# Kernel optimization log

Hardware: AMD Instinct MI355X
Metric: run time of the kernel (lower is better)

The kernel has to match this reference:

```python
import jax, jax.numpy as jnp
import numpy as np

B, S, E, H = 64, 256, 512, 1024  # batch, seq_len, embed, hidden (dis_size=[512,1024,1024])


def _ln(x, g, b, eps=1e-5):
    # LayerNorm over last axis; x: [..., 3, H], g/b: [3, H] (per-gate affine)
    m = x.mean(-1, keepdims=True)
    v = ((x - m) ** 2).mean(-1, keepdims=True)
    return (x - m) * jax.lax.rsqrt(v + eps) * g + b


def _gru_cell(h, x, Wih, Whh, bih, bhh, gig, gib, ghg, ghb):
    Bsz = x.shape[0]
    Hh = h.shape[1]
    pi = _ln((x @ Wih.T + bih).reshape(Bsz, 3, Hh), gig, gib)
    ph = _ln((h @ Whh.T + bhh).reshape(Bsz, 3, Hh), ghg, ghb)
    r = jax.nn.sigmoid(pi[:, 0] + ph[:, 0])
    z = jax.nn.sigmoid(pi[:, 1] + ph[:, 1])
    n = jnp.tanh(pi[:, 2] + r * ph[:, 2])
    return (1.0 - z) * n + z * h


def _unroll(x, layers, W_out, b_out):
    # x: [B, S, E] -> scalar score per batch element from last hidden state
    xs = jnp.swapaxes(x, 0, 1)  # [S, B, E]
    for (Wih, Whh, bih, bhh, gig, gib, ghg, ghb) in layers:
        h0 = jnp.zeros((x.shape[0], Whh.shape[1]), x.dtype)

        def step(h, xt, Wih=Wih, Whh=Whh, bih=bih, bhh=bhh, gig=gig, gib=gib, ghg=ghg, ghb=ghb):
            h2 = _gru_cell(h, xt, Wih, Whh, bih, bhh, gig, gib, ghg, ghb)
            return h2, h2

        _, xs = jax.lax.scan(step, h0, xs)  # xs becomes [S, B, H]
    return (xs[-1] @ W_out.T + b_out)[:, 0]  # [B]


def setup_inputs() -> dict:
    key = jax.random.key(0)
    ks = jax.random.split(key, 12)
    sizes = [(E, H), (H, H)]  # (input_size, hidden_size) per layer
    inp = {
        "generated_data": jax.random.normal(ks[0], (B, S, E), jnp.float32),
        "true_data": jax.random.normal(ks[1], (B, S, E), jnp.float32),
    }
    for li, (ins, hs) in enumerate(sizes):
        k = jax.random.split(ks[2 + li], 4)
        inp[f"W_ih{li}"] = jax.random.normal(k[0], (3 * hs, ins), jnp.float32) * 0.02
        inp[f"W_hh{li}"] = jax.random.normal(k[1], (3 * hs, hs), jnp.float32) * 0.02
        inp[f"b_ih{li}"] = jnp.zeros((3 * hs,), jnp.float32)
        inp[f"b_hh{li}"] = jnp.zeros((3 * hs,), jnp.float32)
        inp[f"gi_g{li}"] = jnp.ones((3, hs), jnp.float32)
        inp[f"gi_b{li}"] = jnp.zeros((3, hs), jnp.float32)
        inp[f"gh_g{li}"] = jnp.ones((3, hs), jnp.float32)
        inp[f"gh_b{li}"] = jnp.zeros((3, hs), jnp.float32)
    inp["W_out"] = jax.random.normal(ks[10], (1, H), jnp.float32) * 0.02
    inp["b_out"] = jnp.zeros((1,), jnp.float32)
    return inp


def reference(generated_data, true_data,
              W_ih0, W_hh0, b_ih0, b_hh0, gi_g0, gi_b0, gh_g0, gh_b0,
              W_ih1, W_hh1, b_ih1, b_hh1, gi_g1, gi_b1, gh_g1, gh_b1,
              W_out, b_out):
    layers = [
        (W_ih0, W_hh0, b_ih0, b_hh0, gi_g0, gi_b0, gh_g0, gh_b0),
        (W_ih1, W_hh1, b_ih1, b_hh1, gi_g1, gi_b1, gh_g1, gh_b1),
    ]
    true_labels = _unroll(true_data, layers, W_out, b_out)
    gen_labels = _unroll(generated_data, layers, W_out, b_out)
    discriminator_loss = -true_labels.mean() + gen_labels.mean()
    generator_loss = -gen_labels.mean()
    return (discriminator_loss, generator_loss)
```

## Files before the change

kernel.cpp:

```cpp
#include <hip/hip_runtime.h>
#include <math.h>

#define NCH   128
#define SLEN  256
#define HDIM  1024
#define N3    3072

typedef __attribute__((ext_vector_type(8))) __bf16 bf16x8;
typedef __attribute__((ext_vector_type(4))) float  f32x4;

__device__ __forceinline__ f32x4 mfma_bf16(bf16x8 a, bf16x8 b, f32x4 c) {
  return __builtin_amdgcn_mfma_f32_16x16x32_bf16(a, b, c, 0, 0, 0);
}

__device__ __forceinline__ float ld_sc1_f32(const float* p) {
  return __hip_atomic_load(p, __ATOMIC_RELAXED, __HIP_MEMORY_SCOPE_AGENT);
}
__device__ __forceinline__ void st_sc1_f32(float* p, float v) {
  __hip_atomic_store(p, v, __ATOMIC_RELAXED, __HIP_MEMORY_SCOPE_AGENT);
}
__device__ __forceinline__ unsigned long long ld_sc1_u64(const unsigned long long* p) {
  return __hip_atomic_load(p, __ATOMIC_RELAXED, __HIP_MEMORY_SCOPE_AGENT);
}
__device__ __forceinline__ void st_sc1_u32(unsigned int* p, unsigned int v) {
  __hip_atomic_store(p, v, __ATOMIC_RELAXED, __HIP_MEMORY_SCOPE_AGENT);
}
__device__ __forceinline__ int ld_sc1_i32(const int* p) {
  return __hip_atomic_load(p, __ATOMIC_RELAXED, __HIP_MEMORY_SCOPE_AGENT);
}
__device__ __forceinline__ void st_sc1_i32(int* p, int v) {
  __hip_atomic_store(p, v, __ATOMIC_RELAXED, __HIP_MEMORY_SCOPE_AGENT);
}

__global__ __launch_bounds__(256) void prep(
    const float* __restrict__ Whh0, const float* __restrict__ Whh1,
    const float* __restrict__ Wih1, const float* __restrict__ Wih0,
    __bf16* __restrict__ Whh0h, __bf16* __restrict__ Whh0l,
    __bf16* __restrict__ Whh1h, __bf16* __restrict__ Whh1l,
    __bf16* __restrict__ Wih1h, __bf16* __restrict__ Wih1l,
    __bf16* __restrict__ Wih0h, __bf16* __restrict__ Wih0l,
    unsigned int* __restrict__ Hpk,
    int* __restrict__ flags)
{
  const int NB = N3 * HDIM;
  const int NS = N3 * 512;
  int i = blockIdx.x * 256 + threadIdx.x;
  const float* src; __bf16 *dh, *dl; int j;
  if (i < NB)            { src = Whh0; dh = Whh0h; dl = Whh0l; j = i; }
  else if (i < 2 * NB)   { src = Whh1; dh = Whh1h; dl = Whh1l; j = i - NB; }
  else if (i < 3 * NB)   { src = Wih1; dh = Wih1h; dl = Wih1l; j = i - 2 * NB; }
  else if (i < 3 * NB + NS) { src = Wih0; dh = Wih0h; dl = Wih0l; j = i - 3 * NB; }
  else if (i < 3 * NB + NS + 2 * NCH * HDIM) { Hpk[i - 3 * NB - NS] = 0u; return; }
  else if (i < 3 * NB + NS + 2 * NCH * HDIM + 512) {
    flags[i - 3 * NB - NS - 2 * NCH * HDIM] = 0; return;
  }
  else return;
  float x = src[j];
  __bf16 h = (__bf16)x;
  dh[j] = h;
  dl[j] = (__bf16)(x - (float)h);
}

__global__ __launch_bounds__(256) void xproj_mfma(
    const float* __restrict__ A0, const float* __restrict__ A1,
    int chainsA0, int strideChain, int t0, int K, int lTc,
    const __bf16* __restrict__ Wh, const __bf16* __restrict__ Wl,
    const float* __restrict__ bias, float* __restrict__ out)
{
  __shared__ __bf16 Ah[4][128][8];
  __shared__ __bf16 Al[4][128][8];
  const int tid  = threadIdx.x;
  const int n0   = blockIdx.x * 128;
  const int row0 = blockIdx.y * 128;
  const int lane = tid & 63;
  const int wv   = tid >> 6;
  const int q    = lane >> 4;
  const int c15  = lane & 15;
  const int m_off = wv * 32;
  const int sr  = tid >> 1;
  const int sq0 = (tid & 1) * 2;
  const int sk  = (tid & 1) * 16;
  const int r     = row0 + sr;
  const int chain = r >> lTc;
  const int dt    = r & ((1 << lTc) - 1);
  const float* aptr = (chain < chainsA0)
      ? (A0 + ((size_t)chain * strideChain + t0 + dt) * K)
      : (A1 + ((size_t)(chain - chainsA0) * strideChain + t0 + dt) * K);

  f32x4 acc[2][8];
#pragma unroll
  for (int i = 0; i < 2; ++i)
#pragma unroll
    for (int j = 0; j < 8; ++j) acc[i][j] = (f32x4){0.f, 0.f, 0.f, 0.f};

  for (int k0 = 0; k0 < K; k0 += 32) {
    float f[16];
    *(float4*)(f + 0)  = *(const float4*)(aptr + k0 + sk + 0);
    *(float4*)(f + 4)  = *(const float4*)(aptr + k0 + sk + 4);
    *(float4*)(f + 8)  = *(const float4*)(aptr + k0 + sk + 8);
    *(float4*)(f + 12) = *(const float4*)(aptr + k0 + sk + 12);
    bf16x8 hv0, hv1, lv0, lv1;
#pragma unroll
    for (int e = 0; e < 8; ++e) {
      __bf16 h0 = (__bf16)f[e];
      hv0[e] = h0;  lv0[e] = (__bf16)(f[e] - (float)h0);
      __bf16 h1 = (__bf16)f[8 + e];
      hv1[e] = h1;  lv1[e] = (__bf16)(f[8 + e] - (float)h1);
    }
    __syncthreads();
    *(bf16x8*)&Ah[sq0][sr][0]     = hv0;
    *(bf16x8*)&Ah[sq0 + 1][sr][0] = hv1;
    *(bf16x8*)&Al[sq0][sr][0]     = lv0;
    *(bf16x8*)&Al[sq0 + 1][sr][0] = lv1;
    __syncthreads();

    bf16x8 a_h[2], a_l[2];
#pragma unroll
    for (int i = 0; i < 2; ++i) {
      a_h[i] = *(const bf16x8*)&Ah[q][m_off + i * 16 + c15][0];
      a_l[i] = *(const bf16x8*)&Al[q][m_off + i * 16 + c15][0];
    }
#pragma unroll
    for (int j = 0; j < 8; ++j) {
      const size_t woff = (size_t)(n0 + j * 16 + c15) * K + k0 + q * 8;
      bf16x8 b_h = *(const bf16x8*)(Wh + woff);
      bf16x8 b_l = *(const bf16x8*)(Wl + woff);
#pragma unroll
      for (int i = 0; i < 2; ++i) {
        acc[i][j] = mfma_bf16(a_h[i], b_h, acc[i][j]);
        acc[i][j] = mfma_bf16(a_h[i], b_l, acc[i][j]);
        acc[i][j] = mfma_bf16(a_l[i], b_h, acc[i][j]);
      }
    }
  }

#pragma unroll
  for (int j = 0; j < 8; ++j) {
    const int col = n0 + j * 16 + c15;
    const float bcol = bias[col];
#pragma unroll
    for (int i = 0; i < 2; ++i) {
#pragma unroll
      for (int rr = 0; rr < 4; ++rr) {
        const int m = m_off + i * 16 + q * 4 + rr;
        out[(size_t)(row0 + m) * N3 + col] = acc[i][j][rr] + bcol;
      }
    }
  }
}

__global__ __launch_bounds__(512, 2) void recur_pers(
    const __bf16* __restrict__ Wh, const __bf16* __restrict__ Wl,
    const float* __restrict__ bhh,
    const float* __restrict__ ghw, const float* __restrict__ ghb,
    const float* __restrict__ giw, const float* __restrict__ gib,
    const float* __restrict__ pi,
    unsigned int* __restrict__ Hpk,
    float* __restrict__ h_carry,
    float* __restrict__ hseq,
    float* __restrict__ stats_part,
    int* __restrict__ flag_a, int* __restrict__ flag_b,
    int Tc, int firstChunk, int base)
{
  const int tid  = threadIdx.x;
  const int bid  = blockIdx.x;
  const int gid  = bid >> 5;
  const int ct   = bid & 31;
  const int lane = tid & 63;
  const int w    = tid >> 6;
  const int q    = lane >> 4;
  const int c15  = lane & 15;
  const int m    = tid & 15;
  const int col  = tid >> 4;
  const int ch   = gid * 16 + m;
  const int Hcol = ct * 32 + col;

  __shared__ float red[8 * 6 * 16 * 16];
  __shared__ float sred[8 * 16 * 12];
  __shared__ float sstat[192];

  bf16x8 bh[6][4], bl[6][4];
  const int kw = w * 128;
#pragma unroll
  for (int t = 0; t < 6; ++t) {
    const int gate = t >> 1, half = t & 1;
    const size_t nrow = (size_t)(gate * 1024 + ct * 32 + half * 16 + c15);
#pragma unroll
    for (int kc = 0; kc < 4; ++kc) {
      const size_t off = nrow * HDIM + kw + kc * 32 + q * 8;
      bh[t][kc] = *(const bf16x8*)(Wh + off);
      bl[t][kc] = *(const bf16x8*)(Wl + off);
    }
  }

  const float bias0 = bhh[Hcol], bias1 = bhh[1024 + Hcol], bias2 = bhh[2048 + Hcol];
  const float lw0 = ghw[Hcol], lw1 = ghw[1024 + Hcol], lw2 = ghw[2048 + Hcol];
  const float lb0 = ghb[Hcol], lb1 = ghb[1024 + Hcol], lb2 = ghb[2048 + Hcol];
  const float iw0 = giw[Hcol], iw1 = giw[1024 + Hcol], iw2 = giw[2048 + Hcol];
  const float ib0 = gib[Hcol], ib1 = gib[1024 + Hcol], ib2 = gib[2048 + Hcol];
  float hprev = firstChunk ? 0.f : h_carry[(size_t)ch * HDIM + Hcol];

  const size_t arowbase = (size_t)(gid * 16 + c15) * HDIM;
  float* my_part = stats_part + ((size_t)gid * 32 + ct) * 192;
  const int* fA = flag_a + (gid << 5);
  const int* fB = flag_b + (gid << 5);
  const int pidx = lane & 31;

  for (int dt = 0; dt < Tc; ++dt) {
    const float* pirow = pi + ((size_t)ch * Tc + dt) * N3 + Hcol;
    const float pr = pirow[0], pz = pirow[1024], pn = pirow[2048];

    if (w == 0 && dt > 0) {
      while (true) {
        int v = ld_sc1_i32(fB + pidx);
        if (!__any(v < base + dt)) break;
        __builtin_amdgcn_s_sleep(1);
      }
    }
    __syncthreads();
    __asm__ __volatile__("" ::: "memory");

    f32x4 acc[6];
#pragma unroll
    for (int t = 0; t < 6; ++t) acc[t] = (f32x4){0.f, 0.f, 0.f, 0.f};

    unsigned long long abuf[2][4];
#pragma unroll
    for (int j = 0; j < 4; ++j) {
      abuf[0][j] = ld_sc1_u64((const unsigned long long*)(Hpk + arowbase + kw + 0 * 32 + q * 8) + j);
      abuf[1][j] = ld_sc1_u64((const unsigned long long*)(Hpk + arowbase + kw + 1 * 32 + q * 8) + j);
    }
#pragma unroll
    for (int kc = 0; kc < 4; ++kc) {
      unsigned int u[8];
#pragma unroll
      for (int j = 0; j < 4; ++j) {
        u[2 * j]     = (unsigned int)(abuf[kc & 1][j]);
        u[2 * j + 1] = (unsigned int)(abuf[kc & 1][j] >> 32);
      }
      union { unsigned int d[4]; bf16x8 v; } uah, ual;
#pragma unroll
      for (int d = 0; d < 4; ++d) {
        uah.d[d] = __builtin_amdgcn_perm(u[2 * d + 1], u[2 * d], 0x05040100u);
        ual.d[d] = __builtin_amdgcn_perm(u[2 * d + 1], u[2 * d], 0x07060302u);
      }
      if (kc < 2) {
#pragma unroll
        for (int j = 0; j < 4; ++j)
          abuf[kc & 1][j] = ld_sc1_u64(
              (const unsigned long long*)(Hpk + arowbase + kw + (kc + 2) * 32 + q * 8) + j);
      }
      bf16x8 ah = uah.v, al = ual.v;
#pragma unroll
      for (int t = 0; t < 6; ++t) {
        acc[t] = mfma_bf16(ah, bh[t][kc], acc[t]);
        acc[t] = mfma_bf16(ah, bl[t][kc], acc[t]);
        acc[t] = mfma_bf16(al, bh[t][kc], acc[t]);
      }
    }

#pragma unroll
    for (int t = 0; t < 6; ++t) {
      const int idx = ((w * 6 + t) * 16 + c15) * 16 + q * 4;
      *(f32x4*)&red[idx] = acc[t];
    }
    __syncthreads();

    float phv0 = 0.f, phv1 = 0.f, phv2 = 0.f;
    {
      const int cn = col & 15;
      const int hi = col >> 4;
#pragma unroll
      for (int w8 = 0; w8 < 8; ++w8) {
        phv0 += red[((w8 * 6 + 0 * 2 + hi) * 16 + cn) * 16 + m];
        phv1 += red[((w8 * 6 + 1 * 2 + hi) * 16 + cn) * 16 + m];
        phv2 += red[((w8 * 6 + 2 * 2 + hi) * 16 + cn) * 16 + m];
      }
    }
    phv0 += bias0; phv1 += bias1; phv2 += bias2;

    {
      float s0 = phv0, s1 = phv1, s2 = phv2;
      float q0 = phv0 * phv0, q1 = phv1 * phv1, q2 = phv2 * phv2;
      float s3 = pr, s4 = pz, s5 = pn;
      float q3 = pr * pr, q4 = pz * pz, q5 = pn * pn;
#pragma unroll
      for (int mm = 16; mm <= 32; mm <<= 1) {
        s0 += __shfl_xor(s0, mm); q0 += __shfl_xor(q0, mm);
        s1 += __shfl_xor(s1, mm); q1 += __shfl_xor(q1, mm);
        s2 += __shfl_xor(s2, mm); q2 += __shfl_xor(q2, mm);
        s3 += __shfl_xor(s3, mm); q3 += __shfl_xor(q3, mm);
        s4 += __shfl_xor(s4, mm); q4 += __shfl_xor(q4, mm);
        s5 += __shfl_xor(s5, mm); q5 += __shfl_xor(q5, mm);
      }
      if (lane < 16) {
        const int b = (w * 16 + lane) * 12;
        sred[b + 0] = s0;  sred[b + 1] = q0;
        sred[b + 2] = s1;  sred[b + 3] = q1;
        sred[b + 4] = s2;  sred[b + 5] = q2;
        sred[b + 6] = s3;  sred[b + 7] = q3;
        sred[b + 8] = s4;  sred[b + 9] = q4;
        sred[b + 10] = s5; sred[b + 11] = q5;
      }
    }
    __syncthreads();

    if (tid < 192) {
      const int m12 = tid / 12;
      const int r12 = tid - m12 * 12;
      float v = 0.f;
#pragma unroll
      for (int w8 = 0; w8 < 8; ++w8) v += sred[(w8 * 16 + m12) * 12 + r12];
      st_sc1_f32(&my_part[tid], v);
    }
    __syncthreads();
    if (tid == 0) st_sc1_i32((int*)fA + ct, base + dt + 1);

    if (w == 0) {
      while (true) {
        int v = ld_sc1_i32(fA + pidx);
        if (!__any(v < base + dt + 1)) break;
        __builtin_amdgcn_s_sleep(1);
      }
    }
    __syncthreads();
    __asm__ __volatile__("" ::: "memory");

    {
      const int cidx = tid >> 4;
      const float* sp = stats_part + ((size_t)gid * 32 + cidx) * 192 + m * 12;
      float p0 = ld_sc1_f32(sp + 0),  p1 = ld_sc1_f32(sp + 1),  p2 = ld_sc1_f32(sp + 2);
      float p3 = ld_sc1_f32(sp + 3),  p4 = ld_sc1_f32(sp + 4),  p5 = ld_sc1_f32(sp + 5);
      float p6 = ld_sc1_f32(sp + 6),  p7 = ld_sc1_f32(sp + 7),  p8 = ld_sc1_f32(sp + 8);
      float p9 = ld_sc1_f32(sp + 9),  p10 = ld_sc1_f32(sp + 10), p11 = ld_sc1_f32(sp + 11);
      p0 += __shfl_xor(p0, 16); p1 += __shfl_xor(p1, 16); p2 += __shfl_xor(p2, 16);
      p3 += __shfl_xor(p3, 16); p4 += __shfl_xor(p4, 16); p5 += __shfl_xor(p5, 16);
      p6 += __shfl_xor(p6, 16); p7 += __shfl_xor(p7, 16); p8 += __shfl_xor(p8, 16);
      p9 += __shfl_xor(p9, 16); p10 += __shfl_xor(p10, 16); p11 += __shfl_xor(p11, 16);
      p0 += __shfl_xor(p0, 32); p1 += __shfl_xor(p1, 32); p2 += __shfl_xor(p2, 32);
      p3 += __shfl_xor(p3, 32); p4 += __shfl_xor(p4, 32); p5 += __shfl_xor(p5, 32);
      p6 += __shfl_xor(p6, 32); p7 += __shfl_xor(p7, 32); p8 += __shfl_xor(p8, 32);
      p9 += __shfl_xor(p9, 32); p10 += __shfl_xor(p10, 32); p11 += __shfl_xor(p11, 32);
      if (lane < 16) {
        const int b = w * 200 + lane * 12;
        red[b + 0] = p0;  red[b + 1] = p1;  red[b + 2] = p2;
        red[b + 3] = p3;  red[b + 4] = p4;  red[b + 5] = p5;
        red[b + 6] = p6;  red[b + 7] = p7;  red[b + 8] = p8;
        red[b + 9] = p9;  red[b + 10] = p10; red[b + 11] = p11;
      }
    }
    __syncthreads();
    if (tid < 192) {
      float v = 0.f;
#pragma unroll
      for (int w8 = 0; w8 < 8; ++w8) v += red[w8 * 200 + tid];
      sstat[tid] = v;
    }
    __syncthreads();

    {
      const int b = m * 12;
      const float mh0 = sstat[b + 0] * (1.f / 1024.f);
      const float vh0 = sstat[b + 1] * (1.f / 1024.f) - mh0 * mh0;
      const float mh1 = sstat[b + 2] * (1.f / 1024.f);
      const float vh1 = sstat[b + 3] * (1.f / 1024.f) - mh1 * mh1;
      const float mh2 = sstat[b + 4] * (1.f / 1024.f);
      const float vh2 = sstat[b + 5] * (1.f / 1024.f) - mh2 * mh2;
      const float mi0 = sstat[b + 6] * (1.f / 1024.f);
      const float vi0 = sstat[b + 7] * (1.f / 1024.f) - mi0 * mi0;
      const float mi1 = sstat[b + 8] * (1.f / 1024.f);
      const float vi1 = sstat[b + 9] * (1.f / 1024.f) - mi1 * mi1;
      const float mi2 = sstat[b + 10] * (1.f / 1024.f);
      const float vi2 = sstat[b + 11] * (1.f / 1024.f) - mi2 * mi2;
      const float nh0 = (phv0 - mh0) * rsqrtf(vh0 + 1e-5f) * lw0 + lb0;
      const float nh1 = (phv1 - mh1) * rsqrtf(vh1 + 1e-5f) * lw1 + lb1;
      const float nh2 = (phv2 - mh2) * rsqrtf(vh2 + 1e-5f) * lw2 + lb2;
      const float ni0 = (pr - mi0) * rsqrtf(vi0 + 1e-5f) * iw0 + ib0;
      const float ni1 = (pz - mi1) * rsqrtf(vi1 + 1e-5f) * iw1 + ib1;
      const float ni2 = (pn - mi2) * rsqrtf(vi2 + 1e-5f) * iw2 + ib2;
      const float r  = 1.f / (1.f + expf(-(ni0 + nh0)));
      const float z  = 1.f / (1.f + expf(-(ni1 + nh1)));
      const float nn = tanhf(ni2 + r * nh2);
      const float hn = (1.f - z) * nn + z * hprev;
      hprev = hn;
      const __bf16 hb = (__bf16)hn;
      const __bf16 lo = (__bf16)(hn - (float)hb);
      unsigned short hs, ls;
      __builtin_memcpy(&hs, &hb, 2);
      __builtin_memcpy(&ls, &lo, 2);
      st_sc1_u32(Hpk + (size_t)ch * HDIM + Hcol,
                 (unsigned int)hs | ((unsigned int)ls << 16));
      if (hseq) hseq[((size_t)ch * Tc + dt) * HDIM + Hcol] = hn;
      if (dt == Tc - 1) h_carry[(size_t)ch * HDIM + Hcol] = hn;
    }
    __syncthreads();
    if (tid == 0) st_sc1_i32((int*)fB + ct, base + dt + 1);
  }
}

__global__ __launch_bounds__(1024) void readout(const float* __restrict__ h,
    const float* __restrict__ Wout, const float* __restrict__ bout,
    float* __restrict__ out)
{
  const int tid  = threadIdx.x;
  const int lane = tid & 63;
  const int w    = tid >> 6;
  __shared__ float lab[128];
  __shared__ float rg[2], rt[2];
  const int c  = w * 8 + (lane >> 3);
  const int j0 = (lane & 7) * 128;
  const float* hp = h + (size_t)c * HDIM + j0;
  float s = 0.f;
#pragma unroll
  for (int j = 0; j < 128; j += 4) {
    float4 v  = *(const float4*)(hp + j);
    float4 wv = *(const float4*)(Wout + j0 + j);
    s += v.x * wv.x + v.y * wv.y + v.z * wv.z + v.w * wv.w;
  }
  s += __shfl_xor(s, 1);
  s += __shfl_xor(s, 2);
  s += __shfl_xor(s, 4);
  if ((lane & 7) == 0) lab[c] = s + bout[0];
  __syncthreads();
  if (tid < 128) {
    float v = lab[tid];
    float g = (tid < 64) ? v : 0.f;
    float t = (tid >= 64) ? v : 0.f;
#pragma unroll
    for (int off = 32; off > 0; off >>= 1) {
      g += __shfl_down(g, off);
      t += __shfl_down(t, off);
    }
    if ((tid & 63) == 0) { rg[tid >> 6] = g; rt[tid >> 6] = t; }
  }
  __syncthreads();
  if (tid == 0) {
    float gm = (rg[0] + rg[1]) * (1.f / 64.f);
    float tm = (rt[0] + rt[1]) * (1.f / 64.f);
    out[0] = -tm + gm;
    out[1] = -gm;
  }
}

extern "C" void kernel_launch(void* const* d_in, const int* in_sizes, int n_in,
                              void* d_out, int out_size, void* d_ws, size_t ws_size,
                              hipStream_t stream)
{
  const float* gen  = (const float*)d_in[0];
  const float* tru  = (const float*)d_in[1];
  const float* Wih0 = (const float*)d_in[2];
  const float* Whh0 = (const float*)d_in[3];
  const float* bih0 = (const float*)d_in[4];
  const float* bhh0 = (const float*)d_in[5];
  const float* gig0 = (const float*)d_in[6];
  const float* gib0 = (const float*)d_in[7];
  const float* ghg0 = (const float*)d_in[8];
  const float* ghb0 = (const float*)d_in[9];
  const float* Wih1 = (const float*)d_in[10];
  const float* Whh1 = (const float*)d_in[11];
  const float* bih1 = (const float*)d_in[12];
  const float* bhh1 = (const float*)d_in[13];
  const float* gig1 = (const float*)d_in[14];
  const float* gib1 = (const float*)d_in[15];
  const float* ghg1 = (const float*)d_in[16];
  const float* ghb1 = (const float*)d_in[17];
  const float* Wout = (const float*)d_in[18];
  const float* bout = (const float*)d_in[19];
  float* out = (float*)d_out;

  __bf16* bp = (__bf16*)d_ws;
  __bf16* Whh0h = bp;  bp += (size_t)N3 * HDIM;
  __bf16* Whh0l = bp;  bp += (size_t)N3 * HDIM;
  __bf16* Whh1h = bp;  bp += (size_t)N3 * HDIM;
  __bf16* Whh1l = bp;  bp += (size_t)N3 * HDIM;
  __bf16* Wih1h = bp;  bp += (size_t)N3 * HDIM;
  __bf16* Wih1l = bp;  bp += (size_t)N3 * HDIM;
  __bf16* Wih0h = bp;  bp += (size_t)N3 * 512;
  __bf16* Wih0l = bp;  bp += (size_t)N3 * 512;
  unsigned int* H0pk = (unsigned int*)bp;
  unsigned int* H1pk = H0pk + (size_t)NCH * HDIM;
  const size_t bf16Bytes = ((char*)(H1pk + (size_t)NCH * HDIM)) - (char*)d_ws;

  const size_t fixedF = 2 * (size_t)NCH * HDIM + 8 * 32 * 192 + 1024;
  int Tc = 256;
  while (Tc > 1) {
    size_t needF = (size_t)NCH * Tc * (N3 + HDIM) + fixedF;
    if (bf16Bytes + needF * 4 <= ws_size) break;
    Tc >>= 1;
  }
  int lTc = 0;
  while ((1 << lTc) < Tc) ++lTc;

  float* fp       = (float*)((char*)d_ws + bf16Bytes);
  float* pi_chunk = fp;   fp += (size_t)NCH * Tc * N3;
  float* h0_chunk = fp;   fp += (size_t)NCH * Tc * HDIM;
  float* h_cur0   = fp;   fp += (size_t)NCH * HDIM;
  float* h_cur1   = fp;   fp += (size_t)NCH * HDIM;
  float* stats    = fp;   fp += 8 * 32 * 192;
  int*   flag_a   = (int*)fp;
  int*   flag_b   = flag_a + 256;

  {
    const int total = 3 * (N3 * HDIM) + (N3 * 512) + 2 * NCH * HDIM + 512;
    prep<<<(total + 255) / 256, 256, 0, stream>>>(
        Whh0, Whh1, Wih1, Wih0,
        Whh0h, Whh0l, Whh1h, Whh1l, Wih1h, Wih1l, Wih0h, Wih0l,
        H0pk, flag_a);
  }

  const int nChunks = SLEN / Tc;
  for (int cidx = 0; cidx < nChunks; ++cidx) {
    const int t0 = cidx * Tc;
    const int first = (cidx == 0) ? 1 : 0;
    xproj_mfma<<<dim3(24, Tc), 256, 0, stream>>>(
        gen, tru, 64, SLEN, t0, 512, lTc, Wih0h, Wih0l, bih0, pi_chunk);
    recur_pers<<<256, 512, 0, stream>>>(
        Whh0h, Whh0l, bhh0, ghg0, ghb0, gig0, gib0, pi_chunk, H0pk, h_cur0,
        h0_chunk, stats, flag_a, flag_b, Tc, first, (cidx * 2 + 0) * Tc);
    xproj_mfma<<<dim3(24, Tc), 256, 0, stream>>>(
        h0_chunk, h0_chunk, NCH, Tc, 0, 1024, lTc, Wih1h, Wih1l, bih1, pi_chunk);
    recur_pers<<<256, 512, 0, stream>>>(
        Whh1h, Whh1l, bhh1, ghg1, ghb1, gig1, gib1, pi_chunk, H1pk, h_cur1,
        (float*)nullptr, stats, flag_a, flag_b, Tc, first, (cidx * 2 + 1) * Tc);
  }

  readout<<<1, 1024, 0, stream>>>(h_cur1, Wout, bout, out);
}
```

Measured before the change: 10.09 ms.

## Fuse input projection into persistent GRU recurrence kernel, computing 8 steps per batch

Removes the separate xproj GEMM kernels and the chunked launch loop. Each persistent recurrence block now computes its own slice of the input projection every 8 timesteps, streaming double-buffered weight tiles through shared memory. Inputs are pre-split into packed bf16 hi/lo words in prep, and layer 0's full hidden sequence is stored packed so layer 1 can read it directly. This avoids the fp32 pi and hseq round-trips through global memory and cuts kernel launches, but it adds periodic GEMM work inside the latency-critical serial loop and uses much more shared memory per block.

```diff
diff --git a/kernel.cpp b/kernel.cpp
--- a/kernel.cpp
+++ b/kernel.cpp
@@ -35,133 +35,97 @@
 __global__ __launch_bounds__(256) void prep(
     const float* __restrict__ Whh0, const float* __restrict__ Whh1,
     const float* __restrict__ Wih1, const float* __restrict__ Wih0,
+    const float* __restrict__ gen,  const float* __restrict__ tru,
     __bf16* __restrict__ Whh0h, __bf16* __restrict__ Whh0l,
     __bf16* __restrict__ Whh1h, __bf16* __restrict__ Whh1l,
     __bf16* __restrict__ Wih1h, __bf16* __restrict__ Wih1l,
     __bf16* __restrict__ Wih0h, __bf16* __restrict__ Wih0l,
-    unsigned int* __restrict__ Hpk,
+    unsigned int* __restrict__ xpk,
+    unsigned int* __restrict__ h0s,
+    unsigned int* __restrict__ H1pk,
     int* __restrict__ flags)
 {
   const int NB = N3 * HDIM;
   const int NS = N3 * 512;
+  const int NX = NCH * SLEN * 512;
   int i = blockIdx.x * 256 + threadIdx.x;
-  const float* src; __bf16 *dh, *dl; int j;
-  if (i < NB)            { src = Whh0; dh = Whh0h; dl = Whh0l; j = i; }
-  else if (i < 2 * NB)   { src = Whh1; dh = Whh1h; dl = Whh1l; j = i - NB; }
-  else if (i < 3 * NB)   { src = Wih1; dh = Wih1h; dl = Wih1l; j = i - 2 * NB; }
-  else if (i < 3 * NB + NS) { src = Wih0; dh = Wih0h; dl = Wih0l; j = i - 3 * NB; }
-  else if (i < 3 * NB + NS + 2 * NCH * HDIM) { Hpk[i - 3 * NB - NS] = 0u; return; }
-  else if (i < 3 * NB + NS + 2 * NCH * HDIM + 512) {
-    flags[i - 3 * NB - NS - 2 * NCH * HDIM] = 0; return;
-  }
-  else return;
-  float x = src[j];
-  __bf16 h = (__bf16)x;
-  dh[j] = h;
-  dl[j] = (__bf16)(x - (float)h);
-}
-
-__global__ __launch_bounds__(256) void xproj_mfma(
-    const float* __restrict__ A0, const float* __restrict__ A1,
-    int chainsA0, int strideChain, int t0, int K, int lTc,
-    const __bf16* __restrict__ Wh, const __bf16* __restrict__ Wl,
-    const float* __restrict__ bias, float* __restrict__ out)
+  if (i < 3 * NB + NS) {
+    const float* src; __bf16 *dh, *dl; int j;
+    if (i < NB)            { src = Whh0; dh = Whh0h; dl = Whh0l; j = i; }
+    else if (i < 2 * NB)   { src = Whh1; dh = Whh1h; dl = Whh1l; j = i - NB; }
+    else if (i < 3 * NB)   { src = Wih1; dh = Wih1h; dl = Wih1l; j = i - 2 * NB; }
+    else                   { src = Wih0; dh = Wih0h; dl = Wih0l; j = i - 3 * NB; }
+    float x = src[j];
+    __bf16 h = (__bf16)x;
+    dh[j] = h;
+    dl[j] = (__bf16)(x - (float)h);
+    return;
+  }
+  i -= 3 * NB + NS;
+  if (i < NX) {
+    float x = (i < NX / 2) ? gen[i] : tru[i - NX / 2];
+    __bf16 h = (__bf16)x;
+    __bf16 l = (__bf16)(x - (float)h);
+    unsigned short hs, ls;
+    __builtin_memcpy(&hs, &h, 2);
+    __builtin_memcpy(&ls, &l, 2);
+    xpk[i] = (unsigned int)hs | ((unsigned int)ls << 16);
+    return;
+  }
+  i -= NX;
+  if (i < NCH * HDIM) {
+    int ch = i >> 10, k = i & 1023;
+    h0s[(size_t)ch * (SLEN + 1) * HDIM + k] = 0u;
+    return;
+  }
+  i -= NCH * HDIM;
+  if (i < NCH * HDIM) { H1pk[i] = 0u; return; }
+  i -= NCH * HDIM;
+  if (i < 512) flags[i] = 0;
+}
+
+__device__ __forceinline__ void load_wtile(
+    __bf16* wt, const __bf16* __restrict__ Wph, const __bf16* __restrict__ Wpl,
+    int KIN, int ct, int chunk, int buf, int tid)
 {
-  __shared__ __bf16 Ah[4][128][8];
-  __shared__ __bf16 Al[4][128][8];
-  const int tid  = threadIdx.x;
-  const int n0   = blockIdx.x * 128;
-  const int row0 = blockIdx.y * 128;
-  const int lane = tid & 63;
-  const int wv   = tid >> 6;
-  const int q    = lane >> 4;
-  const int c15  = lane & 15;
-  const int m_off = wv * 32;
-  const int sr  = tid >> 1;
-  const int sq0 = (tid & 1) * 2;
-  const int sk  = (tid & 1) * 16;
-  const int r     = row0 + sr;
-  const int chain = r >> lTc;
-  const int dt    = r & ((1 << lTc) - 1);
-  const float* aptr = (chain < chainsA0)
-      ? (A0 + ((size_t)chain * strideChain + t0 + dt) * K)
-      : (A1 + ((size_t)(chain - chainsA0) * strideChain + t0 + dt) * K);
-
-  f32x4 acc[2][8];
-#pragma unroll
-  for (int i = 0; i < 2; ++i)
-#pragma unroll
-    for (int j = 0; j < 8; ++j) acc[i][j] = (f32x4){0.f, 0.f, 0.f, 0.f};
-
-  for (int k0 = 0; k0 < K; k0 += 32) {
-    float f[16];
-    *(float4*)(f + 0)  = *(const float4*)(aptr + k0 + sk + 0);
-    *(float4*)(f + 4)  = *(const float4*)(aptr + k0 + sk + 4);
-    *(float4*)(f + 8)  = *(const float4*)(aptr + k0 + sk + 8);
-    *(float4*)(f + 12) = *(const float4*)(aptr + k0 + sk + 12);
-    bf16x8 hv0, hv1, lv0, lv1;
-#pragma unroll
-    for (int e = 0; e < 8; ++e) {
-      __bf16 h0 = (__bf16)f[e];
-      hv0[e] = h0;  lv0[e] = (__bf16)(f[e] - (float)h0);
-      __bf16 h1 = (__bf16)f[8 + e];
-      hv1[e] = h1;  lv1[e] = (__bf16)(f[8 + e] - (float)h1);
-    }
-    __syncthreads();
-    *(bf16x8*)&Ah[sq0][sr][0]     = hv0;
-    *(bf16x8*)&Ah[sq0 + 1][sr][0] = hv1;
-    *(bf16x8*)&Al[sq0][sr][0]     = lv0;
-    *(bf16x8*)&Al[sq0 + 1][sr][0] = lv1;
-    __syncthreads();
-
-    bf16x8 a_h[2], a_l[2];
-#pragma unroll
-    for (int i = 0; i < 2; ++i) {
-      a_h[i] = *(const bf16x8*)&Ah[q][m_off + i * 16 + c15][0];
-      a_l[i] = *(const bf16x8*)&Al[q][m_off + i * 16 + c15][0];
-    }
-#pragma unroll
-    for (int j = 0; j < 8; ++j) {
-      const size_t woff = (size_t)(n0 + j * 16 + c15) * K + k0 + q * 8;
-      bf16x8 b_h = *(const bf16x8*)(Wh + woff);
-      bf16x8 b_l = *(const bf16x8*)(Wl + woff);
-#pragma unroll
-      for (int i = 0; i < 2; ++i) {
-        acc[i][j] = mfma_bf16(a_h[i], b_h, acc[i][j]);
-        acc[i][j] = mfma_bf16(a_h[i], b_l, acc[i][j]);
-        acc[i][j] = mfma_bf16(a_l[i], b_h, acc[i][j]);
-      }
-    }
-  }
-
-#pragma unroll
-  for (int j = 0; j < 8; ++j) {
-    const int col = n0 + j * 16 + c15;
-    const float bcol = bias[col];
-#pragma unroll
-    for (int i = 0; i < 2; ++i) {
-#pragma unroll
-      for (int rr = 0; rr < 4; ++rr) {
-        const int m = m_off + i * 16 + q * 4 + rr;
-        out[(size_t)(row0 + m) * N3 + col] = acc[i][j][rr] + bcol;
-      }
-    }
-  }
-}
-
-__global__ __launch_bounds__(512, 2) void recur_pers(
-    const __bf16* __restrict__ Wh, const __bf16* __restrict__ Wl,
-    const float* __restrict__ bhh,
+#pragma unroll
+  for (int it = 0; it < 3; ++it) {
+    const int idx = tid + it * 512;
+    const int part = (idx >= 768) ? 1 : 0;
+    const int rem  = idx - part * 768;
+    const int row96 = rem >> 3;
+    const int c8    = rem & 7;
+    const int gate  = row96 >> 5;
+    const int r32   = row96 & 31;
+    const int t     = gate * 2 + (r32 >> 4);
+    const int r16   = r32 & 15;
+    const size_t grow = (size_t)(gate * 1024 + ct * 32 + r32);
+    const __bf16* src = (part ? Wpl : Wph) + grow * KIN + chunk * 64 + c8 * 8;
+    __bf16* dst = wt + (size_t)(((buf * 2 + part) * 6 + t) * 16 + r16) * 72 + c8 * 8;
+    *(bf16x8*)dst = *(const bf16x8*)src;
+  }
+}
+
+__global__ __launch_bounds__(512, 2) void recur_fused(
+    const __bf16* __restrict__ Wrh, const __bf16* __restrict__ Wrl,
+    const __bf16* __restrict__ Wph, const __bf16* __restrict__ Wpl,
+    const int KIN, const int nchunk,
+    const float* __restrict__ bih, const float* __restrict__ bhh,
+    const float* __restrict__ giw, const float* __restrict__ gib,
     const float* __restrict__ ghw, const float* __restrict__ ghb,
-    const float* __restrict__ giw, const float* __restrict__ gib,
-    const float* __restrict__ pi,
-    unsigned int* __restrict__ Hpk,
-    float* __restrict__ h_carry,
-    float* __restrict__ hseq,
+    const unsigned int* __restrict__ Ain, const size_t inCh, const int inT,
+    const unsigned int* __restrict__ Arec, const size_t recCh, const int recT,
+    unsigned int* __restrict__ Pub, const size_t pubCh, const int pubT,
+    float* __restrict__ hfin,
     float* __restrict__ stats_part,
-    int* __restrict__ flag_a, int* __restrict__ flag_b,
-    int Tc, int firstChunk, int base)
+    int* __restrict__ fAg, int* __restrict__ fBg,
+    const int base)
 {
+  __shared__ float red[15360];
+  __shared__ float pivb[12288];
+  __shared__ float sred[1536];
+  __shared__ float sstat[192];
+
   const int tid  = threadIdx.x;
   const int bid  = blockIdx.x;
   const int gid  = bid >> 5;
@@ -174,41 +138,105 @@
   const int col  = tid >> 4;
   const int ch   = gid * 16 + m;
   const int Hcol = ct * 32 + col;
-
-  __shared__ float red[8 * 6 * 16 * 16];
-  __shared__ float sred[8 * 16 * 12];
-  __shared__ float sstat[192];
-
-  bf16x8 bh[6][4], bl[6][4];
-  const int kw = w * 128;
+  const int chA  = gid * 16 + c15;
+
+  bf16x8 rh[6][4], rl[6][4];
+  const int kwr = w * 128;
 #pragma unroll
   for (int t = 0; t < 6; ++t) {
     const int gate = t >> 1, half = t & 1;
     const size_t nrow = (size_t)(gate * 1024 + ct * 32 + half * 16 + c15);
 #pragma unroll
     for (int kc = 0; kc < 4; ++kc) {
-      const size_t off = nrow * HDIM + kw + kc * 32 + q * 8;
-      bh[t][kc] = *(const bf16x8*)(Wh + off);
-      bl[t][kc] = *(const bf16x8*)(Wl + off);
-    }
-  }
-
-  const float bias0 = bhh[Hcol], bias1 = bhh[1024 + Hcol], bias2 = bhh[2048 + Hcol];
+      const size_t off = nrow * HDIM + kwr + kc * 32 + q * 8;
+      rh[t][kc] = *(const bf16x8*)(Wrh + off);
+      rl[t][kc] = *(const bf16x8*)(Wrl + off);
+    }
+  }
+
+  const float bI0 = bih[Hcol], bI1 = bih[1024 + Hcol], bI2 = bih[2048 + Hcol];
+  const float bH0 = bhh[Hcol], bH1 = bhh[1024 + Hcol], bH2 = bhh[2048 + Hcol];
+  const float iw0 = giw[Hcol], iw1 = giw[1024 + Hcol], iw2 = giw[2048 + Hcol];
+  const float ib0 = gib[Hcol], ib1 = gib[1024 + Hcol], ib2 = gib[2048 + Hcol];
   const float lw0 = ghw[Hcol], lw1 = ghw[1024 + Hcol], lw2 = ghw[2048 + Hcol];
   const float lb0 = ghb[Hcol], lb1 = ghb[1024 + Hcol], lb2 = ghb[2048 + Hcol];
-  const float iw0 = giw[Hcol], iw1 = giw[1024 + Hcol], iw2 = giw[2048 + Hcol];
-  const float ib0 = gib[Hcol], ib1 = gib[1024 + Hcol], ib2 = gib[2048 + Hcol];
-  float hprev = firstChunk ? 0.f : h_carry[(size_t)ch * HDIM + Hcol];
-
-  const size_t arowbase = (size_t)(gid * 16 + c15) * HDIM;
+  float hprev = 0.f;
+
+  const unsigned int* ainb  = Ain + (size_t)chA * inCh;
+  const unsigned int* arecb = Arec + (size_t)chA * recCh + kwr + q * 8;
+  unsigned int* pubp = Pub + (size_t)ch * pubCh + Hcol;
   float* my_part = stats_part + ((size_t)gid * 32 + ct) * 192;
-  const int* fA = flag_a + (gid << 5);
-  const int* fB = flag_b + (gid << 5);
+  int* fA = fAg + (gid << 5);
+  int* fB = fBg + (gid << 5);
   const int pidx = lane & 31;
-
-  for (int dt = 0; dt < Tc; ++dt) {
-    const float* pirow = pi + ((size_t)ch * Tc + dt) * N3 + Hcol;
-    const float pr = pirow[0], pz = pirow[1024], pn = pirow[2048];
+  const int g2 = w >> 1, uh = w & 1;
+
+  for (int dt = 0; dt < SLEN; ++dt) {
+    if ((dt & 7) == 0) {
+      __bf16* wt = (__bf16*)red;
+      f32x4 pacc[2][4];
+#pragma unroll
+      for (int a = 0; a < 2; ++a)
+#pragma unroll
+        for (int b = 0; b < 4; ++b) pacc[a][b] = (f32x4){0.f, 0.f, 0.f, 0.f};
+
+      load_wtile(wt, Wph, Wpl, KIN, ct, 0, 0, tid);
+      __syncthreads();
+      for (int c = 0; c < nchunk; ++c) {
+        if (c + 1 < nchunk) load_wtile(wt, Wph, Wpl, KIN, ct, c + 1, (c + 1) & 1, tid);
+        if (w < 6) {
+          const __bf16* bhi = wt + (size_t)((c & 1) * 2 + 0) * 6912;
+          const __bf16* blo = wt + (size_t)((c & 1) * 2 + 1) * 6912;
+#pragma unroll
+          for (int uu = 0; uu < 4; ++uu) {
+            const unsigned int* ap = ainb + (size_t)(dt + uh * 4 + uu) * inT + c * 64 + q * 8;
+            unsigned long long a8[8];
+#pragma unroll
+            for (int ks = 0; ks < 2; ++ks)
+#pragma unroll
+              for (int j = 0; j < 4; ++j)
+                a8[ks * 4 + j] = ((const unsigned long long*)(ap + ks * 32))[j];
+#pragma unroll
+            for (int ks = 0; ks < 2; ++ks) {
+              unsigned int ua[8];
+#pragma unroll
+              for (int j = 0; j < 4; ++j) {
+                ua[2 * j]     = (unsigned int)a8[ks * 4 + j];
+                ua[2 * j + 1] = (unsigned int)(a8[ks * 4 + j] >> 32);
+              }
+              union { unsigned int d[4]; bf16x8 v; } uah, ual;
+#pragma unroll
+              for (int d = 0; d < 4; ++d) {
+                uah.d[d] = __builtin_amdgcn_perm(ua[2 * d + 1], ua[2 * d], 0x05040100u);
+                ual.d[d] = __builtin_amdgcn_perm(ua[2 * d + 1], ua[2 * d], 0x07060302u);
+              }
+#pragma unroll
+              for (int tt = 0; tt < 2; ++tt) {
+                const int t = g2 * 2 + tt;
+                const size_t bo = (size_t)(t * 16 + c15) * 72 + ks * 32 + q * 8;
+                bf16x8 wbh = *(const bf16x8*)(bhi + bo);
+                bf16x8 wbl = *(const bf16x8*)(blo + bo);
+                pacc[tt][uu] = mfma_bf16(uah.v, wbh, pacc[tt][uu]);
+                pacc[tt][uu] = mfma_bf16(uah.v, wbl, pacc[tt][uu]);
+                pacc[tt][uu] = mfma_bf16(ual.v, wbh, pacc[tt][uu]);
+              }
+            }
+          }
+        }
+        __syncthreads();
+      }
+      if (w < 6) {
+#pragma unroll
+        for (int uu = 0; uu < 4; ++uu)
+#pragma unroll
+          for (int tt = 0; tt < 2; ++tt)
+#pragma unroll
+            for (int rr = 0; rr < 4; ++rr)
+              pivb[(((uh * 4 + uu) * 16 + (q * 4 + rr)) * 3 + g2) * 32 + tt * 16 + c15] =
+                  pacc[tt][uu][rr];
+      }
+      __syncthreads();
+    }
 
     if (w == 0 && dt > 0) {
       while (true) {
@@ -224,11 +252,12 @@
 #pragma unroll
     for (int t = 0; t < 6; ++t) acc[t] = (f32x4){0.f, 0.f, 0.f, 0.f};
 
+    const unsigned int* arow = arecb + (size_t)dt * recT;
     unsigned long long abuf[2][4];
 #pragma unroll
     for (int j = 0; j < 4; ++j) {
-      abuf[0][j] = ld_sc1_u64((const unsigned long long*)(Hpk + arowbase + kw + 0 * 32 + q * 8) + j);
-      abuf[1][j] = ld_sc1_u64((const unsigned long long*)(Hpk + arowbase + kw + 1 * 32 + q * 8) + j);
+      abuf[0][j] = ld_sc1_u64((const unsigned long long*)(arow + 0 * 32) + j);
+      abuf[1][j] = ld_sc1_u64((const unsigned long long*)(arow + 1 * 32) + j);
     }
 #pragma unroll
     for (int kc = 0; kc < 4; ++kc) {
@@ -248,20 +277,20 @@
 #pragma unroll
         for (int j = 0; j < 4; ++j)
           abuf[kc & 1][j] = ld_sc1_u64(
-              (const unsigned long long*)(Hpk + arowbase + kw + (kc + 2) * 32 + q * 8) + j);
+              (const unsigned long long*)(arow + (kc + 2) * 32) + j);
       }
       bf16x8 ah = uah.v, al = ual.v;
 #pragma unroll
       for (int t = 0; t < 6; ++t) {
-        acc[t] = mfma_bf16(ah, bh[t][kc], acc[t]);
-        acc[t] = mfma_bf16(ah, bl[t][kc], acc[t]);
-        acc[t] = mfma_bf16(al, bh[t][kc], acc[t]);
+        acc[t] = mfma_bf16(ah, rh[t][kc], acc[t]);
+        acc[t] = mfma_bf16(ah, rl[t][kc], acc[t]);
+        acc[t] = mfma_bf16(al, rh[t][kc], acc[t]);
       }
     }
 
 #pragma unroll
     for (int t = 0; t < 6; ++t) {
-      const int idx = ((w * 6 + t) * 16 + c15) * 16 + q * 4;
+      const int idx = ((w * 6 + t) * 16 + c15) * 20 + q * 4;
       *(f32x4*)&red[idx] = acc[t];
     }
     __syncthreads();
@@ -272,18 +301,23 @@
       const int hi = col >> 4;
 #pragma unroll
       for (int w8 = 0; w8 < 8; ++w8) {
-        phv0 += red[((w8 * 6 + 0 * 2 + hi) * 16 + cn) * 16 + m];
-        phv1 += red[((w8 * 6 + 1 * 2 + hi) * 16 + cn) * 16 + m];
-        phv2 += red[((w8 * 6 + 2 * 2 + hi) * 16 + cn) * 16 + m];
-      }
-    }
-    phv0 += bias0; phv1 += bias1; phv2 += bias2;
+        phv0 += red[((w8 * 6 + 0 + hi) * 16 + cn) * 20 + m];
+        phv1 += red[((w8 * 6 + 2 + hi) * 16 + cn) * 20 + m];
+        phv2 += red[((w8 * 6 + 4 + hi) * 16 + cn) * 20 + m];
+      }
+    }
+    phv0 += bH0; phv1 += bH1; phv2 += bH2;
+
+    const int u7 = dt & 7;
+    const float piv0 = pivb[((u7 * 16 + m) * 3 + 0) * 32 + col] + bI0;
+    const float piv1 = pivb[((u7 * 16 + m) * 3 + 1) * 32 + col] + bI1;
+    const float piv2 = pivb[((u7 * 16 + m) * 3 + 2) * 32 + col] + bI2;
 
     {
       float s0 = phv0, s1 = phv1, s2 = phv2;
       float q0 = phv0 * phv0, q1 = phv1 * phv1, q2 = phv2 * phv2;
-      float s3 = pr, s4 = pz, s5 = pn;
-      float q3 = pr * pr, q4 = pz * pz, q5 = pn * pn;
+      float s3 = piv0, s4 = piv1, s5 = piv2;
+      float q3 = piv0 * piv0, q4 = piv1 * piv1, q5 = piv2 * piv2;
 #pragma unroll
       for (int mm = 16; mm <= 32; mm <<= 1) {
         s0 += __shfl_xor(s0, mm); q0 += __shfl_xor(q0, mm);
@@ -375,9 +409,9 @@
       const float nh0 = (phv0 - mh0) * rsqrtf(vh0 + 1e-5f) * lw0 + lb0;
       const float nh1 = (phv1 - mh1) * rsqrtf(vh1 + 1e-5f) * lw1 + lb1;
       const float nh2 = (phv2 - mh2) * rsqrtf(vh2 + 1e-5f) * lw2 + lb2;
-      const float ni0 = (pr - mi0) * rsqrtf(vi0 + 1e-5f) * iw0 + ib0;
-      const float ni1 = (pz - mi1) * rsqrtf(vi1 + 1e-5f) * iw1 + ib1;
-      const float ni2 = (pn - mi2) * rsqrtf(vi2 + 1e-5f) * iw2 + ib2;
+      const float ni0 = (piv0 - mi0) * rsqrtf(vi0 + 1e-5f) * iw0 + ib0;
+      const float ni1 = (piv1 - mi1) * rsqrtf(vi1 + 1e-5f) * iw1 + ib1;
+      const float ni2 = (piv2 - mi2) * rsqrtf(vi2 + 1e-5f) * iw2 + ib2;
       const float r  = 1.f / (1.f + expf(-(ni0 + nh0)));
       const float z  = 1.f / (1.f + expf(-(ni1 + nh1)));
       const float nn = tanhf(ni2 + r * nh2);
@@ -388,10 +422,9 @@
       unsigned short hs, ls;
       __builtin_memcpy(&hs, &hb, 2);
       __builtin_memcpy(&ls, &lo, 2);
-      st_sc1_u32(Hpk + (size_t)ch * HDIM + Hcol,
+      st_sc1_u32(pubp + (size_t)dt * pubT,
                  (unsigned int)hs | ((unsigned int)ls << 16));
-      if (hseq) hseq[((size_t)ch * Tc + dt) * HDIM + Hcol] = hn;
-      if (dt == Tc - 1) h_carry[(size_t)ch * HDIM + Hcol] = hn;
+      if (hfin && dt == SLEN - 1) hfin[(size_t)ch * HDIM + Hcol] = hn;
     }
     __syncthreads();
     if (tid == 0) st_sc1_i32((int*)fB + ct, base + dt + 1);
@@ -477,52 +510,41 @@
   __bf16* Wih1l = bp;  bp += (size_t)N3 * HDIM;
   __bf16* Wih0h = bp;  bp += (size_t)N3 * 512;
   __bf16* Wih0l = bp;  bp += (size_t)N3 * 512;
-  unsigned int* H0pk = (unsigned int*)bp;
-  unsigned int* H1pk = H0pk + (size_t)NCH * HDIM;
-  const size_t bf16Bytes = ((char*)(H1pk + (size_t)NCH * HDIM)) - (char*)d_ws;
-
-  const size_t fixedF = 2 * (size_t)NCH * HDIM + 8 * 32 * 192 + 1024;
-  int Tc = 256;
-  while (Tc > 1) {
-    size_t needF = (size_t)NCH * Tc * (N3 + HDIM) + fixedF;
-    if (bf16Bytes + needF * 4 <= ws_size) break;
-    Tc >>= 1;
-  }
-  int lTc = 0;
-  while ((1 << lTc) < Tc) ++lTc;
-
-  float* fp       = (float*)((char*)d_ws + bf16Bytes);
-  float* pi_chunk = fp;   fp += (size_t)NCH * Tc * N3;
-  float* h0_chunk = fp;   fp += (size_t)NCH * Tc * HDIM;
-  float* h_cur0   = fp;   fp += (size_t)NCH * HDIM;
-  float* h_cur1   = fp;   fp += (size_t)NCH * HDIM;
-  float* stats    = fp;   fp += 8 * 32 * 192;
-  int*   flag_a   = (int*)fp;
-  int*   flag_b   = flag_a + 256;
+
+  unsigned int* h0s  = (unsigned int*)bp;
+  unsigned int* H1pk = h0s + (size_t)NCH * (SLEN + 1) * HDIM;
+  unsigned int* xpk  = H1pk + (size_t)NCH * HDIM;
+
+  float* fp     = (float*)(xpk + (size_t)NCH * SLEN * 512);
+  float* h_cur1 = fp;   fp += (size_t)NCH * HDIM;
+  float* stats  = fp;   fp += 8 * 32 * 192;
+  int*   flag_a = (int*)fp;
+  int*   flag_b = flag_a + 256;
 
   {
-    const int total = 3 * (N3 * HDIM) + (N3 * 512) + 2 * NCH * HDIM + 512;
+    const int total = 3 * (N3 * HDIM) + (N3 * 512) + NCH * SLEN * 512
+                      + 2 * NCH * HDIM + 512;
     prep<<<(total + 255) / 256, 256, 0, stream>>>(
-        Whh0, Whh1, Wih1, Wih0,
+        Whh0, Whh1, Wih1, Wih0, gen, tru,
         Whh0h, Whh0l, Whh1h, Whh1l, Wih1h, Wih1l, Wih0h, Wih0l,
-        H0pk, flag_a);
-  }
-
-  const int nChunks = SLEN / Tc;
-  for (int cidx = 0; cidx < nChunks; ++cidx) {
-    const int t0 = cidx * Tc;
-    const int first = (cidx == 0) ? 1 : 0;
-    xproj_mfma<<<dim3(24, Tc), 256, 0, stream>>>(
-        gen, tru, 64, SLEN, t0, 512, lTc, Wih0h, Wih0l, bih0, pi_chunk);
-    recur_pers<<<256, 512, 0, stream>>>(
-        Whh0h, Whh0l, bhh0, ghg0, ghb0, gig0, gib0, pi_chunk, H0pk, h_cur0,
-        h0_chunk, stats, flag_a, flag_b, Tc, first, (cidx * 2 + 0) * Tc);
-    xproj_mfma<<<dim3(24, Tc), 256, 0, stream>>>(
-        h0_chunk, h0_chunk, NCH, Tc, 0, 1024, lTc, Wih1h, Wih1l, bih1, pi_chunk);
-    recur_pers<<<256, 512, 0, stream>>>(
-        Whh1h, Whh1l, bhh1, ghg1, ghb1, gig1, gib1, pi_chunk, H1pk, h_cur1,
-        (float*)nullptr, stats, flag_a, flag_b, Tc, first, (cidx * 2 + 1) * Tc);
-  }
+        xpk, h0s, H1pk, flag_a);
+  }
+
+  recur_fused<<<256, 512, 0, stream>>>(
+      Whh0h, Whh0l, Wih0h, Wih0l, 512, 8,
+      bih0, bhh0, gig0, gib0, ghg0, ghb0,
+      xpk, (size_t)(SLEN * 512), 512,
+      h0s, (size_t)((SLEN + 1) * HDIM), HDIM,
+      h0s + HDIM, (size_t)((SLEN + 1) * HDIM), HDIM,
+      (float*)nullptr, stats, flag_a, flag_b, 0);
+
+  recur_fused<<<256, 512, 0, stream>>>(
+      Whh1h, Whh1l, Wih1h, Wih1l, 1024, 16,
+      bih1, bhh1, gig1, gib1, ghg1, ghb1,
+      h0s + HDIM, (size_t)((SLEN + 1) * HDIM), HDIM,
+      H1pk, (size_t)HDIM, 0,
+      H1pk, (size_t)HDIM, 0,
+      h_cur1, stats, flag_a, flag_b, SLEN);
 
   readout<<<1, 1024, 0, stream>>>(h_cur1, Wout, bout, out);
 }
```

Result: slower. 13.72 ms (+35.9%).
